# Kernel tuning notes

Measured on AMD Instinct MI355X. Metric: run time of the kernel, lower is better.

Reference implementation:

```python
import jax, jax.numpy as jnp
import numpy as np

N_NODES = 100000
N_EDGES = 3200000
N_GRAPHS = 1000
IN_DIM = 10
HIDDEN = 64
N_CLASSES = 2


def setup_inputs() -> dict:
    key = jax.random.key(0)
    ks = jax.random.split(key, 12)
    x = jax.random.normal(ks[0], (N_NODES, IN_DIM), dtype=jnp.float32)
    edge_index = jax.random.randint(ks[1], (2, N_EDGES), 0, N_NODES, dtype=jnp.int64)
    batch = jnp.sort(jax.random.randint(ks[2], (N_NODES,), 0, N_GRAPHS, dtype=jnp.int64))
    def glorot(k, shape):
        lim = float(np.sqrt(6.0 / (shape[0] + shape[1])))
        return jax.random.uniform(k, shape, jnp.float32, -lim, lim)
    W1 = glorot(ks[3], (IN_DIM, HIDDEN)); b1 = jnp.zeros((HIDDEN,), jnp.float32)
    W2 = glorot(ks[4], (HIDDEN, HIDDEN)); b2 = jnp.zeros((HIDDEN,), jnp.float32)
    W3 = glorot(ks[5], (HIDDEN, HIDDEN)); b3 = jnp.zeros((HIDDEN,), jnp.float32)
    Wl = glorot(ks[6], (HIDDEN, N_CLASSES))
    bl = jnp.zeros((N_CLASSES,), jnp.float32)
    return {"x": x, "edge_index": edge_index, "batch": batch,
            "W1": W1, "b1": b1, "W2": W2, "b2": b2, "W3": W3, "b3": b3,
            "Wl": Wl, "bl": bl}


def _gcn_norm(edge_index, n_nodes):
    # PyG gcn_norm with add_self_loops=False: deg computed at target (col)
    row, col = edge_index[0], edge_index[1]
    deg = jax.ops.segment_sum(jnp.ones((edge_index.shape[1],), jnp.float32), col,
                              num_segments=n_nodes)
    dinv = jnp.where(deg > 0, deg ** -0.5, 0.0)
    return dinv[row] * dinv[col]  # [E]


def _gcn_conv(h, W, b, row, col, norm, n_nodes):
    h = h @ W                      # [N, H]
    msg = h[row] * norm[:, None]   # [E, H] gather + edge scale
    agg = jax.ops.segment_sum(msg, col, num_segments=n_nodes)  # scatter-add at target
    return agg + b


def reference(x, edge_index, batch, W1, b1, W2, b2, W3, b3, Wl, bl):
    row, col = edge_index[0], edge_index[1]
    norm = _gcn_norm(edge_index, N_NODES)
    h = jax.nn.relu(_gcn_conv(x, W1, b1, row, col, norm, N_NODES))
    h = jax.nn.relu(_gcn_conv(h, W2, b2, row, col, norm, N_NODES))
    node_embs = _gcn_conv(h, W3, b3, row, col, norm, N_NODES)
    graph_emb = jax.ops.segment_sum(node_embs, batch, num_segments=N_GRAPHS)  # global_add_pool
    # dropout is identity in eval mode
    logits = graph_emb @ Wl + bl
    return jax.nn.softmax(logits, axis=1)
```

## Files before the change

kernel.cpp:

```cpp
#include <hip/hip_runtime.h>

#define N_NODES 100000
#define N_EDGES 3200000
#define N_GRAPHS 1000
#define IN_DIM 10
#define HIDDEN 64

__global__ void k_deg(const int* __restrict__ col, int* __restrict__ deg) {
    int e = blockIdx.x * blockDim.x + threadIdx.x;
    if (e < N_EDGES) atomicAdd(&deg[col[e]], 1);
}

__global__ __launch_bounds__(1024) void k_scan_block(const int* __restrict__ deg,
                                                     int* __restrict__ offs,
                                                     int* __restrict__ bsums) {
    __shared__ int s[1024];
    int t = threadIdx.x;
    int i = blockIdx.x * 1024 + t;
    int v = (i < N_NODES) ? deg[i] : 0;
    s[t] = v;
    __syncthreads();
    for (int d = 1; d < 1024; d <<= 1) {
        int x = (t >= d) ? s[t - d] : 0;
        __syncthreads();
        s[t] += x;
        __syncthreads();
    }
    if (i < N_NODES) offs[i] = s[t] - v;
    if (t == 1023) bsums[blockIdx.x] = s[t];
}

__global__ __launch_bounds__(128) void k_scan_top(int* __restrict__ bsums, int nb) {
    __shared__ int s[128];
    int t = threadIdx.x;
    int v = (t < nb) ? bsums[t] : 0;
    s[t] = v;
    __syncthreads();
    for (int d = 1; d < 128; d <<= 1) {
        int x = (t >= d) ? s[t - d] : 0;
        __syncthreads();
        s[t] += x;
        __syncthreads();
    }
    if (t < nb) bsums[t] = s[t] - v;
}

__global__ __launch_bounds__(1024) void k_scan_add(int* __restrict__ offs,
                                                   const int* __restrict__ bsums) {
    int i = blockIdx.x * 1024 + threadIdx.x;
    if (i < N_NODES) offs[i] += bsums[blockIdx.x];
}

__global__ void k_dinv(const int* __restrict__ deg, float* __restrict__ dinv) {
    int n = blockIdx.x * blockDim.x + threadIdx.x;
    if (n < N_NODES) {
        int d = deg[n];
        dinv[n] = (d > 0) ? rsqrtf((float)d) : 0.f;
    }
}

__global__ void k_fill(const int* __restrict__ row, const int* __restrict__ col,
                       const int* __restrict__ offs, int* __restrict__ cursor,
                       int* __restrict__ csr_src) {
    int e = blockIdx.x * blockDim.x + threadIdx.x;
    if (e < N_EDGES) {
        int d = col[e];
        int p = atomicAdd(&cursor[d], 1);
        csr_src[offs[d] + p] = row[e];
    }
}

__device__ __forceinline__ float agg64(const float* __restrict__ hin,
                                       const float* __restrict__ dinv,
                                       const int* __restrict__ csr_src,
                                       int start, int dn, int lane) {
    float a = 0.f;
    for (int base = 0; base < dn; base += 64) {
        int nb = min(64, dn - base);
        int src = 0;
        float w = 0.f;
        if (lane < nb) {
            src = csr_src[start + base + lane];
            w = dinv[src];
        }
        int j = 0;
        for (; j + 8 <= nb; j += 8) {
            float v0, v1, v2, v3, v4, v5, v6, v7;
            float w0, w1, w2, w3, w4, w5, w6, w7;
            int s0 = __shfl(src, j + 0); w0 = __shfl(w, j + 0);
            int s1 = __shfl(src, j + 1); w1 = __shfl(w, j + 1);
            int s2 = __shfl(src, j + 2); w2 = __shfl(w, j + 2);
            int s3 = __shfl(src, j + 3); w3 = __shfl(w, j + 3);
            int s4 = __shfl(src, j + 4); w4 = __shfl(w, j + 4);
            int s5 = __shfl(src, j + 5); w5 = __shfl(w, j + 5);
            int s6 = __shfl(src, j + 6); w6 = __shfl(w, j + 6);
            int s7 = __shfl(src, j + 7); w7 = __shfl(w, j + 7);
            v0 = hin[s0 * HIDDEN + lane];
            v1 = hin[s1 * HIDDEN + lane];
            v2 = hin[s2 * HIDDEN + lane];
            v3 = hin[s3 * HIDDEN + lane];
            v4 = hin[s4 * HIDDEN + lane];
            v5 = hin[s5 * HIDDEN + lane];
            v6 = hin[s6 * HIDDEN + lane];
            v7 = hin[s7 * HIDDEN + lane];
            a += v0 * w0; a += v1 * w1; a += v2 * w2; a += v3 * w3;
            a += v4 * w4; a += v5 * w5; a += v6 * w6; a += v7 * w7;
        }
        for (; j < nb; ++j) {
            int s = __shfl(src, j);
            float ww = __shfl(w, j);
            a += hin[s * HIDDEN + lane] * ww;
        }
    }
    return a;
}

__global__ __launch_bounds__(256) void k_layer1(const float* __restrict__ x,
                                                const float* __restrict__ dinv,
                                                const int* __restrict__ offs,
                                                const int* __restrict__ deg,
                                                const int* __restrict__ csr_src,
                                                const float* __restrict__ W1,
                                                const float* __restrict__ b1,
                                                float* __restrict__ h1) {
    int wid = (blockIdx.x * blockDim.x + threadIdx.x) >> 6;
    int lane = threadIdx.x & 63;
    if (wid >= N_NODES) return;
    int n = wid;
    int start = offs[n], dn = deg[n];
    float a = 0.f;
    for (int base = 0; base < dn; base += 64) {
        int nb = min(64, dn - base);
        int src = 0;
        float w = 0.f;
        if (lane < nb) {
            src = csr_src[start + base + lane];
            w = dinv[src];
        }
        int j = 0;
        for (; j + 8 <= nb; j += 8) {
            float v0 = 0, v1 = 0, v2 = 0, v3 = 0, v4 = 0, v5 = 0, v6 = 0, v7 = 0;
            int s0 = __shfl(src, j + 0); float w0 = __shfl(w, j + 0);
            int s1 = __shfl(src, j + 1); float w1 = __shfl(w, j + 1);
            int s2 = __shfl(src, j + 2); float w2 = __shfl(w, j + 2);
            int s3 = __shfl(src, j + 3); float w3 = __shfl(w, j + 3);
            int s4 = __shfl(src, j + 4); float w4 = __shfl(w, j + 4);
            int s5 = __shfl(src, j + 5); float w5 = __shfl(w, j + 5);
            int s6 = __shfl(src, j + 6); float w6 = __shfl(w, j + 6);
            int s7 = __shfl(src, j + 7); float w7 = __shfl(w, j + 7);
            if (lane < IN_DIM) {
                v0 = x[s0 * IN_DIM + lane];
                v1 = x[s1 * IN_DIM + lane];
                v2 = x[s2 * IN_DIM + lane];
                v3 = x[s3 * IN_DIM + lane];
                v4 = x[s4 * IN_DIM + lane];
                v5 = x[s5 * IN_DIM + lane];
                v6 = x[s6 * IN_DIM + lane];
                v7 = x[s7 * IN_DIM + lane];
            }
            a += v0 * w0; a += v1 * w1; a += v2 * w2; a += v3 * w3;
            a += v4 * w4; a += v5 * w5; a += v6 * w6; a += v7 * w7;
        }
        for (; j < nb; ++j) {
            int s = __shfl(src, j);
            float ww = __shfl(w, j);
            if (lane < IN_DIM) a += x[s * IN_DIM + lane] * ww;
        }
    }
    a *= dinv[n];
    float acc = b1[lane];
#pragma unroll
    for (int k = 0; k < IN_DIM; ++k) {
        acc += __shfl(a, k) * W1[k * HIDDEN + lane];
    }
    h1[n * HIDDEN + lane] = fmaxf(acc, 0.f);
}

__global__ __launch_bounds__(256) void k_layer2(const float* __restrict__ hin,
                                                const float* __restrict__ dinv,
                                                const int* __restrict__ offs,
                                                const int* __restrict__ deg,
                                                const int* __restrict__ csr_src,
                                                const float* __restrict__ W,
                                                const float* __restrict__ b,
                                                float* __restrict__ hout) {
    __shared__ float sW[HIDDEN * HIDDEN];
    for (int i = threadIdx.x; i < HIDDEN * HIDDEN; i += blockDim.x) sW[i] = W[i];
    __syncthreads();
    int wid = (blockIdx.x * blockDim.x + threadIdx.x) >> 6;
    int lane = threadIdx.x & 63;
    if (wid >= N_NODES) return;
    int n = wid;
    float a = agg64(hin, dinv, csr_src, offs[n], deg[n], lane);
    a *= dinv[n];
    float acc = b[lane];
    for (int k = 0; k < HIDDEN; ++k) {
        acc += __shfl(a, k) * sW[k * HIDDEN + lane];
    }
    hout[n * HIDDEN + lane] = fmaxf(acc, 0.f);
}

__global__ __launch_bounds__(256) void k_layer3(const float* __restrict__ hin,
                                                const float* __restrict__ dinv,
                                                const int* __restrict__ offs,
                                                const int* __restrict__ deg,
                                                const int* __restrict__ csr_src,
                                                const int* __restrict__ batch,
                                                float* __restrict__ gpre,
                                                int* __restrict__ gcnt) {
    int wid = (blockIdx.x * blockDim.x + threadIdx.x) >> 6;
    int lane = threadIdx.x & 63;
    if (wid >= N_NODES) return;
    int n = wid;
    float a = agg64(hin, dinv, csr_src, offs[n], deg[n], lane);
    a *= dinv[n];
    int g = batch[n];
    atomicAdd(&gpre[g * HIDDEN + lane], a);
    if (lane == 0) atomicAdd(&gcnt[g], 1);
}

__global__ __launch_bounds__(256) void k_final(const float* __restrict__ gpre,
                                               const int* __restrict__ gcnt,
                                               const float* __restrict__ W3,
                                               const float* __restrict__ b3,
                                               const float* __restrict__ Wl,
                                               const float* __restrict__ bl,
                                               float* __restrict__ out) {
    int wid = (blockIdx.x * blockDim.x + threadIdx.x) >> 6;
    int lane = threadIdx.x & 63;
    if (wid >= N_GRAPHS) return;
    float pre = gpre[wid * HIDDEN + lane];
    float cnt = (float)gcnt[wid];
    float emb = cnt * b3[lane];
    for (int k = 0; k < HIDDEN; ++k) {
        emb += __shfl(pre, k) * W3[k * HIDDEN + lane];
    }
    float p0 = emb * Wl[lane * 2 + 0];
    float p1 = emb * Wl[lane * 2 + 1];
    for (int d = 32; d > 0; d >>= 1) {
        p0 += __shfl_xor(p0, d);
        p1 += __shfl_xor(p1, d);
    }
    if (lane == 0) {
        float l0 = p0 + bl[0], l1 = p1 + bl[1];
        float m = fmaxf(l0, l1);
        float e0 = __expf(l0 - m), e1 = __expf(l1 - m);
        float inv = 1.f / (e0 + e1);
        out[wid * 2 + 0] = e0 * inv;
        out[wid * 2 + 1] = e1 * inv;
    }
}

extern "C" void kernel_launch(void* const* d_in, const int* in_sizes, int n_in,
                              void* d_out, int out_size, void* d_ws, size_t ws_size,
                              hipStream_t stream) {
    const float* x = (const float*)d_in[0];
    const int* edge = (const int*)d_in[1];
    const int* batch = (const int*)d_in[2];
    const float* W1 = (const float*)d_in[3];
    const float* b1 = (const float*)d_in[4];
    const float* W2 = (const float*)d_in[5];
    const float* b2 = (const float*)d_in[6];
    const float* W3 = (const float*)d_in[7];
    const float* b3 = (const float*)d_in[8];
    const float* Wl = (const float*)d_in[9];
    const float* bl = (const float*)d_in[10];
    float* out = (float*)d_out;

    const int* row = edge;
    const int* col = edge + N_EDGES;

    char* ws = (char*)d_ws;
    size_t off = 0;
    auto alloc = [&](size_t bytes) -> void* {
        void* p = ws + off;
        off = (off + bytes + 255) & ~(size_t)255;
        return p;
    };
    int* deg = (int*)alloc((size_t)N_NODES * 4);
    int* offs = (int*)alloc((size_t)N_NODES * 4);
    int* bsums = (int*)alloc(128 * 4);
    int* cursor = (int*)alloc((size_t)N_NODES * 4);
    float* dinv = (float*)alloc((size_t)N_NODES * 4);
    int* csr_src = (int*)alloc((size_t)N_EDGES * 4);
    float* h1 = (float*)alloc((size_t)N_NODES * HIDDEN * 4);
    float* h2 = (float*)alloc((size_t)N_NODES * HIDDEN * 4);
    float* gpre = (float*)alloc((size_t)N_GRAPHS * HIDDEN * 4);
    int* gcnt = (int*)alloc((size_t)N_GRAPHS * 4);

    hipMemsetAsync(deg, 0, (size_t)N_NODES * 4, stream);
    hipMemsetAsync(cursor, 0, (size_t)N_NODES * 4, stream);
    hipMemsetAsync(gpre, 0, (size_t)N_GRAPHS * HIDDEN * 4, stream);
    hipMemsetAsync(gcnt, 0, (size_t)N_GRAPHS * 4, stream);

    const int EB = (N_EDGES + 255) / 256;
    const int NB1024 = (N_NODES + 1023) / 1024;

    k_deg<<<EB, 256, 0, stream>>>(col, deg);
    k_scan_block<<<NB1024, 1024, 0, stream>>>(deg, offs, bsums);
    k_scan_top<<<1, 128, 0, stream>>>(bsums, NB1024);
    k_scan_add<<<NB1024, 1024, 0, stream>>>(offs, bsums);
    k_dinv<<<(N_NODES + 255) / 256, 256, 0, stream>>>(deg, dinv);
    k_fill<<<EB, 256, 0, stream>>>(row, col, offs, cursor, csr_src);

    const int WB = (N_NODES * 64 + 255) / 256;
    k_layer1<<<WB, 256, 0, stream>>>(x, dinv, offs, deg, csr_src, W1, b1, h1);
    k_layer2<<<WB, 256, 0, stream>>>(h1, dinv, offs, deg, csr_src, W2, b2, h2);
    k_layer3<<<WB, 256, 0, stream>>>(h2, dinv, offs, deg, csr_src, batch, gpre, gcnt);
    k_final<<<(N_GRAPHS * 64 + 255) / 256, 256, 0, stream>>>(gpre, gcnt, W3, b3, Wl, bl, out);
}
```

Baseline: 815.5 us.

## Partition CSR fill by destination range to localize scatter writes

The CSR fill kernel now launches 8 blocks per 4096-edge chunk. Each block reads the whole chunk but only handles edges whose target node falls in its own eighth of the node range. This keeps atomic cursor updates and csr_src writes confined to a smaller address window per block, aiming for better cache locality of the random scatter. In exchange, every edge's row and col are read 8 times, and each thread does a strided loop of 16 edges.

```diff
diff --git a/kernel.cpp b/kernel.cpp
--- a/kernel.cpp
+++ b/kernel.cpp
@@ -5,6 +5,10 @@
 #define N_GRAPHS 1000
 #define IN_DIM 10
 #define HIDDEN 64
+
+#define NRANGES 8
+#define RANGE_SIZE ((N_NODES + NRANGES - 1) / NRANGES)
+#define CHUNK_EDGES 4096
 
 __global__ void k_deg(const int* __restrict__ col, int* __restrict__ deg) {
     int e = blockIdx.x * blockDim.x + threadIdx.x;
@@ -59,14 +63,27 @@
     }
 }
 
-__global__ void k_fill(const int* __restrict__ row, const int* __restrict__ col,
-                       const int* __restrict__ offs, int* __restrict__ cursor,
-                       int* __restrict__ csr_src) {
-    int e = blockIdx.x * blockDim.x + threadIdx.x;
-    if (e < N_EDGES) {
-        int d = col[e];
-        int p = atomicAdd(&cursor[d], 1);
-        csr_src[offs[d] + p] = row[e];
+__global__ __launch_bounds__(256) void k_fill(const int* __restrict__ row,
+                                              const int* __restrict__ col,
+                                              const int* __restrict__ offs,
+                                              int* __restrict__ cursor,
+                                              int* __restrict__ csr_src) {
+    int range = blockIdx.x & (NRANGES - 1);
+    int chunk = blockIdx.x >> 3;
+    int lo = range * RANGE_SIZE;
+    int hi = lo + RANGE_SIZE;
+    int base = chunk * CHUNK_EDGES + threadIdx.x;
+#pragma unroll
+    for (int k = 0; k < CHUNK_EDGES / 256; ++k) {
+        int e = base + k * 256;
+        if (e < N_EDGES) {
+            int c = col[e];
+            int r = row[e];
+            if (c >= lo && c < hi) {
+                int p = atomicAdd(&cursor[c], 1);
+                csr_src[offs[c] + p] = r;
+            }
+        }
     }
 }
 
@@ -301,7 +318,9 @@
     k_scan_top<<<1, 128, 0, stream>>>(bsums, NB1024);
     k_scan_add<<<NB1024, 1024, 0, stream>>>(offs, bsums);
     k_dinv<<<(N_NODES + 255) / 256, 256, 0, stream>>>(deg, dinv);
-    k_fill<<<EB, 256, 0, stream>>>(row, col, offs, cursor, csr_src);
+
+    const int NCHUNKS = (N_EDGES + CHUNK_EDGES - 1) / CHUNK_EDGES;
+    k_fill<<<NCHUNKS * NRANGES, 256, 0, stream>>>(row, col, offs, cursor, csr_src);
 
     const int WB = (N_NODES * 64 + 255) / 256;
     k_layer1<<<WB, 256, 0, stream>>>(x, dinv, offs, deg, csr_src, W1, b1, h1);
```

Result: faster. 746.9 us (-8.4%).
